# Optimization experiments

Measured on AMD Instinct MI355X. Metric: run time of the kernel, lower is better.

The kernel has to match this reference:

```python
import jax, jax.numpy as jnp
import numpy as np

TEMPERATURE = 8.0  # sqrt(d_head=64)
NEG_INF = -1e15


def setup_inputs() -> dict:
    key = jax.random.key(0)
    k1, k2_, k3, k4, k5, k6 = jax.random.split(key, 6)
    BH, N, D = 16, 2048, 64
    B = 2  # edge batch; BH // B == 8 heads
    return {
        "q": jax.random.normal(k1, (BH, N, D), dtype=jnp.float32),
        "k": jax.random.normal(k2_, (BH, N, D), dtype=jnp.float32),
        "v": jax.random.normal(k3, (BH, N, D), dtype=jnp.float32),
        "k2": jax.random.normal(k4, (BH, N, D), dtype=jnp.float32),
        "mask": jax.random.randint(k5, (BH, 1, N), 0, 2) > 0,
        "edge": jax.random.randint(k6, (B, N, N), 0, 2).astype(jnp.int32),
    }


def reference(q, k, v, k2, mask, edge):
    # attn scores: [bh, n, m]
    attn = jnp.einsum("bnd,bmd->bnm", q, k) / TEMPERATURE
    # torch .repeat along dim0 == tile
    reps = attn.shape[0] // edge.shape[0]
    edge_t = jnp.tile(edge, (reps, 1, 1))
    attn = jnp.where(edge_t == 0, NEG_INF, attn)
    attn = jnp.where(mask, NEG_INF, attn)
    attn = jax.nn.softmax(attn, axis=2)  # dropout p=0 (eval)
    output = jnp.einsum("bnm,bmd->bnd", attn, v)
    # non_linear=False, so no sigmoid
    return (output, attn)
```

## Files before the change

kernel.cpp:

```cpp
#include <hip/hip_runtime.h>
#include <stdint.h>
#include <math.h>

#define BH_ 16
#define N_  2048
#define D_  64
#define NEGV (-1e15f)

typedef __attribute__((ext_vector_type(8))) short bf16x8;
typedef __attribute__((ext_vector_type(8))) unsigned short us8;
typedef __attribute__((ext_vector_type(4))) float f32x4;

#define OFF_MASKU8 0u
#define OFF_MBITS  32768u
#define OFF_EBITS  65536u
#define OFF_QBF    1114112u
#define OFF_KBF    5308416u
#define OFF_VT     9502720u
#define WS_NEEDED  13697024u

#define BARRIER_LGKM() do {                                   \
    asm volatile("s_waitcnt lgkmcnt(0)" ::: "memory");        \
    __builtin_amdgcn_sched_barrier(0);                        \
    __builtin_amdgcn_s_barrier();                             \
    __builtin_amdgcn_sched_barrier(0);                        \
} while (0)

__device__ __forceinline__ unsigned short f2bf(float f) {
    unsigned u = __float_as_uint(f);
    return (unsigned short)((u + 0x7FFFu + ((u >> 16) & 1u)) >> 16);
}

__global__ __launch_bounds__(256)
void prep_all(const float* __restrict__ q, const float* __restrict__ k,
              const float* __restrict__ v, const void* __restrict__ mraw,
              const int* __restrict__ edge,
              unsigned short* __restrict__ qbf, unsigned short* __restrict__ kbf,
              unsigned short* __restrict__ vT,
              unsigned short* __restrict__ e16, unsigned long long* __restrict__ mbits)
{
    __shared__ unsigned short shbuf[64][72];
    __shared__ int flag;
    const int bid = blockIdx.x;
    const int t   = threadIdx.x;

    if (bid < 2048) {
        const int idx = bid * 256 + t;
        const int4* p = (const int4*)(edge + (size_t)idx * 16);
        unsigned m = 0;
        #pragma unroll
        for (int i = 0; i < 4; ++i) {
            const int4 vv = p[i];
            m |= (vv.x != 0 ? 1u : 0u) << (i * 4 + 0);
            m |= (vv.y != 0 ? 1u : 0u) << (i * 4 + 1);
            m |= (vv.z != 0 ? 1u : 0u) << (i * 4 + 2);
            m |= (vv.w != 0 ? 1u : 0u) << (i * 4 + 3);
        }
        e16[idx] = (unsigned short)m;
    } else if (bid < 2560) {
        const int b2 = bid - 2048;
        const int rt = b2 & 31, bh = b2 >> 5;
        const size_t base = ((size_t)bh * N_ + (size_t)rt * 64) * D_;
        #pragma unroll
        for (int i = 0; i < 4; ++i) {
            const int idx = t + i * 256;
            float4 f = *(const float4*)(q + base + (size_t)idx * 4);
            ushort4 s; s.x = f2bf(f.x); s.y = f2bf(f.y); s.z = f2bf(f.z); s.w = f2bf(f.w);
            *(ushort4*)(qbf + base + (size_t)idx * 4) = s;
            f = *(const float4*)(k + base + (size_t)idx * 4);
            s.x = f2bf(f.x); s.y = f2bf(f.y); s.z = f2bf(f.z); s.w = f2bf(f.w);
            *(ushort4*)(kbf + base + (size_t)idx * 4) = s;
            f = *(const float4*)(v + base + (size_t)idx * 4);
            const int row = idx >> 4;
            const int d0  = (idx & 15) * 4;
            shbuf[d0 + 0][row] = f2bf(f.x);
            shbuf[d0 + 1][row] = f2bf(f.y);
            shbuf[d0 + 2][row] = f2bf(f.z);
            shbuf[d0 + 3][row] = f2bf(f.w);
        }
        __syncthreads();
        const int d  = t >> 2;
        const int c4 = (t & 3) * 16;
        const size_t ob = ((size_t)bh * D_ + d) * N_ + (size_t)rt * 64 + c4;
        *(us8*)(vT + ob)     = *(us8*)&shbuf[d][c4];
        *(us8*)(vT + ob + 8) = *(us8*)&shbuf[d][c4 + 8];
    } else {
        const int bh = bid - 2560;
        if (t == 0) flag = 0;
        __syncthreads();
        const int* mi = (const int*)mraw;
        int bad = 0;
        for (int i = t; i < 8192; i += 256)
            if ((unsigned)mi[i] > 1u) bad = 1;
        if (bad) atomicOr(&flag, 1);
        __syncthreads();
        const int is_u8 = flag;
        const uint8_t* m8 = (const uint8_t*)mraw;
        const int w4 = t >> 6, l = t & 63;
        for (int it = 0; it < 8; ++it) {
            const int pos = bh * 2048 + it * 256 + w4 * 64 + l;
            const bool on = is_u8 ? (m8[pos] != 0) : (mi[pos] != 0);
            unsigned long long bal = __ballot(on);
            if (l == 0) mbits[bh * 32 + it * 4 + w4] = bal;
        }
    }
}

__global__ __launch_bounds__(256)
void attn_v6(const unsigned short* __restrict__ qbf,
             const unsigned short* __restrict__ kbf,
             const unsigned short* __restrict__ vT,
             const unsigned long long* __restrict__ ebits,
             const unsigned long long* __restrict__ mbits,
             float* __restrict__ out, float* __restrict__ attn)
{
    __shared__ unsigned short sK[2][4096];
    __shared__ unsigned short sV[2][4096];
    __shared__ char pbuf[4][2048];

    const int tile = blockIdx.x;
    const int bh   = blockIdx.y;
    const int t    = threadIdx.x;
    const int w    = t >> 6;
    const int lane = t & 63;
    const int l15  = lane & 15;
    const int lg   = lane >> 4;
    const int rbase = tile * 64;
    const int myrow = rbase + w * 16 + l15;

    const unsigned short* qb = qbf + (size_t)bh * N_ * D_;
    const unsigned short* kb = kbf + (size_t)bh * N_ * D_;
    const unsigned short* vb = vT  + (size_t)bh * D_ * N_;
    const unsigned long long* ebrow =
        ebits + ((size_t)(bh & 1) * N_ + (size_t)myrow) * 32;
    const unsigned long long* mb = mbits + bh * 32;
    float* outb = out + (size_t)bh * N_ * D_;
    float* arow = attn + (size_t)bh * N_ * N_ + (size_t)myrow * N_ + lg * 4;

    const bf16x8 aq0 = *(const bf16x8*)(qb + (size_t)myrow * D_ + lg * 8);
    const bf16x8 aq1 = *(const bf16x8*)(qb + (size_t)myrow * D_ + lg * 8 + 32);

    const int s0row = t >> 3;
    const int s1row = s0row + 32;
    const int t8    = t & 7;
    const int ds0 = s0row * 64 + ((t8 ^ (s0row & 7)) * 8);
    const int ds1 = s1row * 64 + ((t8 ^ (s1row & 7)) * 8);

    {
        const us8 a0 = *(const us8*)(kb + (size_t)t * 8);
        const us8 a1 = *(const us8*)(kb + (size_t)(t + 256) * 8);
        *(us8*)(sK[0] + ds0) = a0;
        *(us8*)(sK[0] + ds1) = a1;
        BARRIER_LGKM();
    }
    float lacc = 0.f;
    #pragma unroll 1
    for (int kc = 0; kc < 32; ++kc) {
        const int cur = kc & 1;
        us8 nk0, nk1;
        if (kc < 31) {
            const unsigned short* s = kb + (size_t)(kc + 1) * 4096;
            nk0 = *(const us8*)(s + (size_t)t * 8);
            nk1 = *(const us8*)(s + (size_t)(t + 256) * 8);
        }
        const unsigned long long wbits = ebrow[kc] & ~mb[kc];
        const unsigned short* kcur = sK[cur];
        #pragma unroll
        for (int nt = 0; nt < 4; ++nt) {
            const int row = nt * 16 + l15, sw = row & 7;
            const bf16x8 k0 = *(const bf16x8*)(kcur + row * 64 + ((lg ^ sw) * 8));
            const bf16x8 k1 = *(const bf16x8*)(kcur + row * 64 + (((lg + 4) ^ sw) * 8));
            f32x4 c = (f32x4){0.f, 0.f, 0.f, 0.f};
            c = __builtin_amdgcn_mfma_f32_16x16x32_bf16(k0, aq0, c, 0, 0, 0);
            c = __builtin_amdgcn_mfma_f32_16x16x32_bf16(k1, aq1, c, 0, 0, 0);
            const unsigned bits = (unsigned)(wbits >> (nt * 16 + lg * 4)) & 0xFu;
            #pragma unroll
            for (int r = 0; r < 4; ++r)
                lacc += ((bits >> r) & 1u) ? __expf(c[r] * 0.125f) : 0.f;
        }
        if (kc < 31) {
            *(us8*)(sK[cur ^ 1] + ds0) = nk0;
            *(us8*)(sK[cur ^ 1] + ds1) = nk1;
        }
        BARRIER_LGKM();
    }
    lacc += __shfl_xor(lacc, 16);
    lacc += __shfl_xor(lacc, 32);
    const float inv = 1.0f / lacc;

    {
        const us8 a0 = *(const us8*)(kb + (size_t)t * 8);
        const us8 a1 = *(const us8*)(kb + (size_t)(t + 256) * 8);
        const us8 b0 = *(const us8*)(vb + (size_t)s0row * 2048 + t8 * 8);
        const us8 b1 = *(const us8*)(vb + (size_t)s1row * 2048 + t8 * 8);
        *(us8*)(sK[0] + ds0) = a0;
        *(us8*)(sK[0] + ds1) = a1;
        *(us8*)(sV[0] + ds0) = b0;
        *(us8*)(sV[0] + ds1) = b1;
        BARRIER_LGKM();
    }

    f32x4 o[4];
    #pragma unroll
    for (int nt = 0; nt < 4; ++nt) o[nt] = (f32x4){0.f, 0.f, 0.f, 0.f};

    char* pbw = pbuf[w];
    const int swzP = (l15 & 7) << 4;
    const int ab0 = (l15 * 128 + lg * 16)      ^ swzP;
    const int ab1 = (l15 * 128 + lg * 16 + 64) ^ swzP;

    #pragma unroll 1
    for (int kc = 0; kc < 32; ++kc) {
        const int cur = kc & 1;
        us8 nk0, nk1, nv0, nv1;
        if (kc < 31) {
            const unsigned short* srck = kb + (size_t)(kc + 1) * 4096;
            const unsigned short* srcv = vb + (size_t)(kc + 1) * 64;
            nk0 = *(const us8*)(srck + (size_t)t * 8);
            nk1 = *(const us8*)(srck + (size_t)(t + 256) * 8);
            nv0 = *(const us8*)(srcv + (size_t)s0row * 2048 + t8 * 8);
            nv1 = *(const us8*)(srcv + (size_t)s1row * 2048 + t8 * 8);
        }
        const unsigned long long wbits = ebrow[kc] & ~mb[kc];
        const unsigned short* kcur = sK[cur];
        float4 ev[4];
        #pragma unroll
        for (int nt = 0; nt < 4; ++nt) {
            const int row = nt * 16 + l15, sw = row & 7;
            const bf16x8 k0 = *(const bf16x8*)(kcur + row * 64 + ((lg ^ sw) * 8));
            const bf16x8 k1 = *(const bf16x8*)(kcur + row * 64 + (((lg + 4) ^ sw) * 8));
            f32x4 c = (f32x4){0.f, 0.f, 0.f, 0.f};
            c = __builtin_amdgcn_mfma_f32_16x16x32_bf16(k0, aq0, c, 0, 0, 0);
            c = __builtin_amdgcn_mfma_f32_16x16x32_bf16(k1, aq1, c, 0, 0, 0);
            const unsigned bits = (unsigned)(wbits >> (nt * 16 + lg * 4)) & 0xFu;
            float4 e;
            e.x = (bits & 1u) ? __expf(c[0] * 0.125f) * inv : 0.f;
            e.y = (bits & 2u) ? __expf(c[1] * 0.125f) * inv : 0.f;
            e.z = (bits & 4u) ? __expf(c[2] * 0.125f) * inv : 0.f;
            e.w = (bits & 8u) ? __expf(c[3] * 0.125f) * inv : 0.f;
            ev[nt] = e;
            ushort4 pe;
            pe.x = f2bf(e.x); pe.y = f2bf(e.y); pe.z = f2bf(e.z); pe.w = f2bf(e.w);
            const int wbyte = (l15 * 128 + nt * 32 + lg * 8) ^ swzP;
            *(ushort4*)(pbw + wbyte) = pe;
        }
        const bf16x8 ap0 = *(const bf16x8*)(pbw + ab0);
        const bf16x8 ap1 = *(const bf16x8*)(pbw + ab1);
        const unsigned short* vcur = sV[cur];
        #pragma unroll
        for (int nt = 0; nt < 4; ++nt) {
            const int row = nt * 16 + l15, sw = row & 7;
            const bf16x8 bv0 = *(const bf16x8*)(vcur + row * 64 + ((lg ^ sw) * 8));
            const bf16x8 bv1 = *(const bf16x8*)(vcur + row * 64 + (((lg + 4) ^ sw) * 8));
            o[nt] = __builtin_amdgcn_mfma_f32_16x16x32_bf16(ap0, bv0, o[nt], 0, 0, 0);
            o[nt] = __builtin_amdgcn_mfma_f32_16x16x32_bf16(ap1, bv1, o[nt], 0, 0, 0);
        }
        {
            float* astore = arow + kc * 64;
            #pragma unroll
            for (int nt = 0; nt < 4; ++nt)
                *(float4*)(astore + nt * 16) = ev[nt];
        }
        if (kc < 31) {
            *(us8*)(sK[cur ^ 1] + ds0) = nk0;
            *(us8*)(sK[cur ^ 1] + ds1) = nk1;
            *(us8*)(sV[cur ^ 1] + ds0) = nv0;
            *(us8*)(sV[cur ^ 1] + ds1) = nv1;
        }
        BARRIER_LGKM();
    }

    #pragma unroll
    for (int nt = 0; nt < 4; ++nt)
        #pragma unroll
        for (int r = 0; r < 4; ++r)
            outb[(size_t)(rbase + w * 16 + lg * 4 + r) * D_ + nt * 16 + l15] = o[nt][r];
}

__global__ __launch_bounds__(256)
void normalize_mask(const void* __restrict__ mask_raw, uint8_t* __restrict__ mask_out)
{
    __shared__ int is_u8;
    const int t = threadIdx.x;
    if (t == 0) is_u8 = 0;
    __syncthreads();
    const int* mi = (const int*)mask_raw;
    int bad = 0;
    for (int i = t; i < 8192; i += 256)
        if ((unsigned)mi[i] > 1u) bad = 1;
    if (bad) atomicOr(&is_u8, 1);
    __syncthreads();
    const int total = BH_ * N_;
    if (is_u8) {
        const uint8_t* m8 = (const uint8_t*)mask_raw;
        for (int i = t; i < total; i += 256) mask_out[i] = m8[i] ? 1 : 0;
    } else {
        for (int i = t; i < total; i += 256) mask_out[i] = (uint8_t)mi[i];
    }
}

__global__ __launch_bounds__(256)
void attn_fused(const float* __restrict__ q, const float* __restrict__ k,
                const float* __restrict__ v, const uint8_t* __restrict__ mask,
                const int* __restrict__ edge, float* __restrict__ out,
                float* __restrict__ attn)
{
    __shared__ float qsT[D_][64 + 4];
    __shared__ float kt [D_][64 + 4];
    __shared__ float vs [64][D_ + 4];
    const int tile = blockIdx.x, bh = blockIdx.y, t = threadIdx.x;
    const int rg = t >> 4, cg = t & 15, r0 = rg * 4, c0 = cg * 4;
    const int row_base = tile * 64;
    const float* qb = q + (size_t)bh * N_ * D_;
    const float* kb = k + (size_t)bh * N_ * D_;
    const float* vb = v + (size_t)bh * N_ * D_;
    const uint8_t* mbp = mask + (size_t)bh * N_;
    const int* ebp = edge + (size_t)(bh & 1) * N_ * N_;
    float* outb = out + (size_t)bh * N_ * D_;
    float* attnb = attn + (size_t)bh * N_ * N_;
    {
        const int rr = t >> 2, dblk = (t & 3) * 16;
        const float* src = qb + (size_t)(row_base + rr) * D_ + dblk;
        #pragma unroll
        for (int qq = 0; qq < 4; ++qq) {
            float4 val = *(const float4*)(src + qq * 4);
            qsT[dblk + qq*4 + 0][rr] = val.x; qsT[dblk + qq*4 + 1][rr] = val.y;
            qsT[dblk + qq*4 + 2][rr] = val.z; qsT[dblk + qq*4 + 3][rr] = val.w;
        }
    }
    float m_i[4], l_i[4];
    #pragma unroll
    for (int i = 0; i < 4; ++i) { m_i[i] = -INFINITY; l_i[i] = 0.f; }
    for (int kc = 0; kc < 32; ++kc) {
        __syncthreads();
        {
            const int ccr = t >> 2, dblk = (t & 3) * 16;
            const float* src = kb + (size_t)(kc * 64 + ccr) * D_ + dblk;
            #pragma unroll
            for (int qq = 0; qq < 4; ++qq) {
                float4 val = *(const float4*)(src + qq * 4);
                kt[dblk + qq*4 + 0][ccr] = val.x; kt[dblk + qq*4 + 1][ccr] = val.y;
                kt[dblk + qq*4 + 2][ccr] = val.z; kt[dblk + qq*4 + 3][ccr] = val.w;
            }
        }
        __syncthreads();
        float sc[4][4];
        #pragma unroll
        for (int i = 0; i < 4; ++i) { sc[i][0]=sc[i][1]=sc[i][2]=sc[i][3]=0.f; }
        for (int d = 0; d < D_; ++d) {
            const float4 qv = *(const float4*)&qsT[d][r0];
            const float4 kv = *(const float4*)&kt[d][c0];
            #pragma unroll
            for (int i = 0; i < 4; ++i) {
                const float qi = (i==0)?qv.x:(i==1)?qv.y:(i==2)?qv.z:qv.w;
                sc[i][0] = fmaf(qi, kv.x, sc[i][0]); sc[i][1] = fmaf(qi, kv.y, sc[i][1]);
                sc[i][2] = fmaf(qi, kv.z, sc[i][2]); sc[i][3] = fmaf(qi, kv.w, sc[i][3]);
            }
        }
        const int cbase = kc * 64 + c0;
        const uint8_t m0 = mbp[cbase], m1 = mbp[cbase+1], m2 = mbp[cbase+2], m3 = mbp[cbase+3];
        #pragma unroll
        for (int i = 0; i < 4; ++i) {
            const int rglob = row_base + r0 + i;
            const int4 e4 = *(const int4*)(ebp + (size_t)rglob * N_ + cbase);
            float s0 = sc[i][0]*0.125f, s1 = sc[i][1]*0.125f, s2 = sc[i][2]*0.125f, s3 = sc[i][3]*0.125f;
            if (e4.x == 0 || m0) s0 = NEGV; if (e4.y == 0 || m1) s1 = NEGV;
            if (e4.z == 0 || m2) s2 = NEGV; if (e4.w == 0 || m3) s3 = NEGV;
            float cmax = fmaxf(fmaxf(s0,s1), fmaxf(s2,s3));
            cmax = fmaxf(cmax, __shfl_xor(cmax,1)); cmax = fmaxf(cmax, __shfl_xor(cmax,2));
            cmax = fmaxf(cmax, __shfl_xor(cmax,4)); cmax = fmaxf(cmax, __shfl_xor(cmax,8));
            const float nm = fmaxf(m_i[i], cmax);
            float ss = __expf(s0-nm)+__expf(s1-nm)+__expf(s2-nm)+__expf(s3-nm);
            ss += __shfl_xor(ss,1); ss += __shfl_xor(ss,2); ss += __shfl_xor(ss,4); ss += __shfl_xor(ss,8);
            l_i[i] = l_i[i]*__expf(m_i[i]-nm) + ss; m_i[i] = nm;
        }
    }
    float inv_l[4];
    #pragma unroll
    for (int i = 0; i < 4; ++i) inv_l[i] = 1.0f / l_i[i];
    float oacc[4][4];
    #pragma unroll
    for (int i = 0; i < 4; ++i) { oacc[i][0]=oacc[i][1]=oacc[i][2]=oacc[i][3]=0.f; }
    for (int kc = 0; kc < 32; ++kc) {
        __syncthreads();
        {
            const int ccr = t >> 2, dblk = (t & 3) * 16;
            const float* src = kb + (size_t)(kc * 64 + ccr) * D_ + dblk;
            #pragma unroll
            for (int qq = 0; qq < 4; ++qq) {
                float4 val = *(const float4*)(src + qq * 4);
                kt[dblk + qq*4 + 0][ccr] = val.x; kt[dblk + qq*4 + 1][ccr] = val.y;
                kt[dblk + qq*4 + 2][ccr] = val.z; kt[dblk + qq*4 + 3][ccr] = val.w;
            }
            const float* srcv = vb + (size_t)(kc * 64 + ccr) * D_ + dblk;
            #pragma unroll
            for (int qq = 0; qq < 4; ++qq)
                *(float4*)&vs[ccr][dblk + qq * 4] = *(const float4*)(srcv + qq * 4);
        }
        __syncthreads();
        float sc[4][4];
        #pragma unroll
        for (int i = 0; i < 4; ++i) { sc[i][0]=sc[i][1]=sc[i][2]=sc[i][3]=0.f; }
        for (int d = 0; d < D_; ++d) {
            const float4 qv = *(const float4*)&qsT[d][r0];
            const float4 kv = *(const float4*)&kt[d][c0];
            #pragma unroll
            for (int i = 0; i < 4; ++i) {
                const float qi = (i==0)?qv.x:(i==1)?qv.y:(i==2)?qv.z:qv.w;
                sc[i][0] = fmaf(qi, kv.x, sc[i][0]); sc[i][1] = fmaf(qi, kv.y, sc[i][1]);
                sc[i][2] = fmaf(qi, kv.z, sc[i][2]); sc[i][3] = fmaf(qi, kv.w, sc[i][3]);
            }
        }
        const int cbase = kc * 64 + c0;
        const uint8_t m0 = mbp[cbase], m1 = mbp[cbase+1], m2 = mbp[cbase+2], m3 = mbp[cbase+3];
        float p[4][4];
        #pragma unroll
        for (int i = 0; i < 4; ++i) {
            const int rglob = row_base + r0 + i;
            const int4 e4 = *(const int4*)(ebp + (size_t)rglob * N_ + cbase);
            float s0 = sc[i][0]*0.125f, s1 = sc[i][1]*0.125f, s2 = sc[i][2]*0.125f, s3 = sc[i][3]*0.125f;
            if (e4.x == 0 || m0) s0 = NEGV; if (e4.y == 0 || m1) s1 = NEGV;
            if (e4.z == 0 || m2) s2 = NEGV; if (e4.w == 0 || m3) s3 = NEGV;
            p[i][0] = __expf(s0-m_i[i])*inv_l[i]; p[i][1] = __expf(s1-m_i[i])*inv_l[i];
            p[i][2] = __expf(s2-m_i[i])*inv_l[i]; p[i][3] = __expf(s3-m_i[i])*inv_l[i];
            *(float4*)&attnb[(size_t)rglob * N_ + cbase] = make_float4(p[i][0],p[i][1],p[i][2],p[i][3]);
        }
        __syncthreads();
        #pragma unroll
        for (int i = 0; i < 4; ++i)
            *(float4*)&kt[r0 + i][c0] = make_float4(p[i][0],p[i][1],p[i][2],p[i][3]);
        __syncthreads();
        for (int c4 = 0; c4 < 64; c4 += 4) {
            float prr[4][4];
            #pragma unroll
            for (int i = 0; i < 4; ++i) {
                const float4 tmp = *(const float4*)&kt[r0 + i][c4];
                prr[i][0]=tmp.x; prr[i][1]=tmp.y; prr[i][2]=tmp.z; prr[i][3]=tmp.w;
            }
            #pragma unroll
            for (int cc = 0; cc < 4; ++cc) {
                const float4 vv = *(const float4*)&vs[c4 + cc][c0];
                #pragma unroll
                for (int i = 0; i < 4; ++i) {
                    oacc[i][0] = fmaf(prr[i][cc], vv.x, oacc[i][0]);
                    oacc[i][1] = fmaf(prr[i][cc], vv.y, oacc[i][1]);
                    oacc[i][2] = fmaf(prr[i][cc], vv.z, oacc[i][2]);
                    oacc[i][3] = fmaf(prr[i][cc], vv.w, oacc[i][3]);
                }
            }
        }
    }
    #pragma unroll
    for (int i = 0; i < 4; ++i)
        *(float4*)&outb[(size_t)(row_base + r0 + i) * D_ + c0] =
            make_float4(oacc[i][0], oacc[i][1], oacc[i][2], oacc[i][3]);
}

extern "C" void kernel_launch(void* const* d_in, const int* in_sizes, int n_in,
                              void* d_out, int out_size, void* d_ws, size_t ws_size,
                              hipStream_t stream) {
    const float* q    = (const float*)d_in[0];
    const float* k    = (const float*)d_in[1];
    const float* v    = (const float*)d_in[2];
    const void*  mraw = d_in[4];
    const int*   edge = (const int*)d_in[5];

    float* out  = (float*)d_out;
    float* attn = (float*)d_out + (size_t)BH_ * N_ * D_;

    char* ws = (char*)d_ws;

    if (ws_size < (size_t)WS_NEEDED) {
        uint8_t* mask_u8 = (uint8_t*)(ws + OFF_MASKU8);
        normalize_mask<<<1, 256, 0, stream>>>(mraw, mask_u8);
        attn_fused<<<dim3(32, 16), 256, 0, stream>>>(q, k, v, mask_u8, edge, out, attn);
        return;
    }

    unsigned long long* mbits = (unsigned long long*)(ws + OFF_MBITS);
    unsigned short*     e16   = (unsigned short*)(ws + OFF_EBITS);
    unsigned short*     qbf   = (unsigned short*)(ws + OFF_QBF);
    unsigned short*     kbf   = (unsigned short*)(ws + OFF_KBF);
    unsigned short*     vT    = (unsigned short*)(ws + OFF_VT);

    prep_all<<<dim3(2576), 256, 0, stream>>>(q, k, v, mraw, edge,
                                             qbf, kbf, vT, e16, mbits);
    attn_v6<<<dim3(N_ / 64, BH_), 256, 0, stream>>>(
        qbf, kbf, vT, (const unsigned long long*)e16, mbits, out, attn);
}
```

Baseline: 127.8 us.

## Split attention into row-sum, split-K PV pass, and output reduction kernels

Replaces the single attention kernel with three kernels. A first pass computes softmax denominators over four key splits. A second pass, split two ways over keys, writes normalized probabilities and partial outputs, and a final kernel sums the two partial outputs. The aim is more blocks in flight (512 → 2048/1024) to fill the GPU. The cost is recomputing QK^T, extra workspace traffic for the partial outputs and row sums, and two more launches. The softmax skips max subtraction, which relies on scores staying small enough not to overflow exp.

```diff
diff --git a/kernel.cpp b/kernel.cpp
--- a/kernel.cpp
+++ b/kernel.cpp
@@ -17,7 +17,10 @@
 #define OFF_QBF    1114112u
 #define OFF_KBF    5308416u
 #define OFF_VT     9502720u
-#define WS_NEEDED  13697024u
+#define WS_V6      13697024u
+#define OFF_PSUM   13697024u
+#define OFF_OPART  14221312u
+#define WS_V7      30998528u
 
 #define BARRIER_LGKM() do {                                   \
     asm volatile("s_waitcnt lgkmcnt(0)" ::: "memory");        \
@@ -104,6 +107,219 @@
             if (l == 0) mbits[bh * 32 + it * 4 + w4] = bal;
         }
     }
+}
+
+__global__ __launch_bounds__(256)
+void attn_sumk(const unsigned short* __restrict__ qbf,
+               const unsigned short* __restrict__ kbf,
+               const unsigned long long* __restrict__ ebits,
+               const unsigned long long* __restrict__ mbits,
+               float* __restrict__ psum)
+{
+    __shared__ unsigned short sK[2][4096];
+
+    const int tile = blockIdx.x, bh = blockIdx.y, s = blockIdx.z;
+    const int t = threadIdx.x;
+    const int w = t >> 6, lane = t & 63, l15 = lane & 15, lg = lane >> 4;
+    const int rbase = tile * 64;
+    const int myrow = rbase + w * 16 + l15;
+    const int kcb = s * 8;
+
+    const unsigned short* qb = qbf + (size_t)bh * N_ * D_;
+    const unsigned short* kb = kbf + (size_t)bh * N_ * D_;
+    const unsigned long long* ebrow =
+        ebits + ((size_t)(bh & 1) * N_ + (size_t)myrow) * 32;
+    const unsigned long long* mb = mbits + bh * 32;
+
+    const bf16x8 aq0 = *(const bf16x8*)(qb + (size_t)myrow * D_ + lg * 8);
+    const bf16x8 aq1 = *(const bf16x8*)(qb + (size_t)myrow * D_ + lg * 8 + 32);
+
+    const int s0row = t >> 3, s1row = s0row + 32, t8 = t & 7;
+    const int ds0 = s0row * 64 + ((t8 ^ (s0row & 7)) * 8);
+    const int ds1 = s1row * 64 + ((t8 ^ (s1row & 7)) * 8);
+
+    {
+        const unsigned short* src = kb + (size_t)kcb * 4096;
+        *(us8*)(sK[0] + ds0) = *(const us8*)(src + (size_t)t * 8);
+        *(us8*)(sK[0] + ds1) = *(const us8*)(src + (size_t)(t + 256) * 8);
+        BARRIER_LGKM();
+    }
+    float lacc = 0.f;
+    #pragma unroll 1
+    for (int i = 0; i < 8; ++i) {
+        const int kc = kcb + i;
+        const int cur = i & 1;
+        us8 nk0, nk1;
+        if (i < 7) {
+            const unsigned short* src = kb + (size_t)(kc + 1) * 4096;
+            nk0 = *(const us8*)(src + (size_t)t * 8);
+            nk1 = *(const us8*)(src + (size_t)(t + 256) * 8);
+        }
+        const unsigned long long wbits = ebrow[kc] & ~mb[kc];
+        const unsigned short* kcur = sK[cur];
+        #pragma unroll
+        for (int nt = 0; nt < 4; ++nt) {
+            const int row = nt * 16 + l15, sw = row & 7;
+            const bf16x8 k0 = *(const bf16x8*)(kcur + row * 64 + ((lg ^ sw) * 8));
+            const bf16x8 k1 = *(const bf16x8*)(kcur + row * 64 + (((lg + 4) ^ sw) * 8));
+            f32x4 c = (f32x4){0.f, 0.f, 0.f, 0.f};
+            c = __builtin_amdgcn_mfma_f32_16x16x32_bf16(k0, aq0, c, 0, 0, 0);
+            c = __builtin_amdgcn_mfma_f32_16x16x32_bf16(k1, aq1, c, 0, 0, 0);
+            const unsigned bits = (unsigned)(wbits >> (nt * 16 + lg * 4)) & 0xFu;
+            #pragma unroll
+            for (int r = 0; r < 4; ++r)
+                lacc += ((bits >> r) & 1u) ? __expf(c[r] * 0.125f) : 0.f;
+        }
+        if (i < 7) {
+            *(us8*)(sK[cur ^ 1] + ds0) = nk0;
+            *(us8*)(sK[cur ^ 1] + ds1) = nk1;
+        }
+        BARRIER_LGKM();
+    }
+    lacc += __shfl_xor(lacc, 16);
+    lacc += __shfl_xor(lacc, 32);
+    if (lane < 16) psum[((size_t)bh * N_ + myrow) * 4 + s] = lacc;
+}
+
+__global__ __launch_bounds__(256)
+void attn_pvk(const unsigned short* __restrict__ qbf,
+              const unsigned short* __restrict__ kbf,
+              const unsigned short* __restrict__ vT,
+              const unsigned long long* __restrict__ ebits,
+              const unsigned long long* __restrict__ mbits,
+              const float* __restrict__ psum,
+              float* __restrict__ opart, float* __restrict__ attn)
+{
+    __shared__ unsigned short sK[2][4096];
+    __shared__ unsigned short sV[2][4096];
+    __shared__ char pbuf[4][2048];
+
+    const int tile = blockIdx.x, bh = blockIdx.y, s = blockIdx.z;
+    const int t = threadIdx.x;
+    const int w = t >> 6, lane = t & 63, l15 = lane & 15, lg = lane >> 4;
+    const int rbase = tile * 64;
+    const int myrow = rbase + w * 16 + l15;
+    const int kcb = s * 16;
+
+    const unsigned short* qb = qbf + (size_t)bh * N_ * D_;
+    const unsigned short* kb = kbf + (size_t)bh * N_ * D_;
+    const unsigned short* vb = vT  + (size_t)bh * D_ * N_;
+    const unsigned long long* ebrow =
+        ebits + ((size_t)(bh & 1) * N_ + (size_t)myrow) * 32;
+    const unsigned long long* mb = mbits + bh * 32;
+    float* arow = attn + (size_t)bh * N_ * N_ + (size_t)myrow * N_ + lg * 4;
+
+    const f32x4 ps = *(const f32x4*)(psum + ((size_t)bh * N_ + myrow) * 4);
+    const float inv = 1.0f / (ps[0] + ps[1] + ps[2] + ps[3]);
+
+    const bf16x8 aq0 = *(const bf16x8*)(qb + (size_t)myrow * D_ + lg * 8);
+    const bf16x8 aq1 = *(const bf16x8*)(qb + (size_t)myrow * D_ + lg * 8 + 32);
+
+    const int s0row = t >> 3, s1row = s0row + 32, t8 = t & 7;
+    const int ds0 = s0row * 64 + ((t8 ^ (s0row & 7)) * 8);
+    const int ds1 = s1row * 64 + ((t8 ^ (s1row & 7)) * 8);
+
+    {
+        const unsigned short* srck = kb + (size_t)kcb * 4096;
+        const unsigned short* srcv = vb + (size_t)kcb * 64;
+        *(us8*)(sK[0] + ds0) = *(const us8*)(srck + (size_t)t * 8);
+        *(us8*)(sK[0] + ds1) = *(const us8*)(srck + (size_t)(t + 256) * 8);
+        *(us8*)(sV[0] + ds0) = *(const us8*)(srcv + (size_t)s0row * 2048 + t8 * 8);
+        *(us8*)(sV[0] + ds1) = *(const us8*)(srcv + (size_t)s1row * 2048 + t8 * 8);
+        BARRIER_LGKM();
+    }
+
+    f32x4 o[4];
+    #pragma unroll
+    for (int nt = 0; nt < 4; ++nt) o[nt] = (f32x4){0.f, 0.f, 0.f, 0.f};
+
+    char* pbw = pbuf[w];
+    const int swzP = (l15 & 7) << 4;
+    const int ab0 = (l15 * 128 + lg * 16)      ^ swzP;
+    const int ab1 = (l15 * 128 + lg * 16 + 64) ^ swzP;
+
+    #pragma unroll 1
+    for (int i = 0; i < 16; ++i) {
+        const int kc = kcb + i;
+        const int cur = i & 1;
+        us8 nk0, nk1, nv0, nv1;
+        if (i < 15) {
+            const unsigned short* srck = kb + (size_t)(kc + 1) * 4096;
+            const unsigned short* srcv = vb + (size_t)(kc + 1) * 64;
+            nk0 = *(const us8*)(srck + (size_t)t * 8);
+            nk1 = *(const us8*)(srck + (size_t)(t + 256) * 8);
+            nv0 = *(const us8*)(srcv + (size_t)s0row * 2048 + t8 * 8);
+            nv1 = *(const us8*)(srcv + (size_t)s1row * 2048 + t8 * 8);
+        }
+        const unsigned long long wbits = ebrow[kc] & ~mb[kc];
+        const unsigned short* kcur = sK[cur];
+        float4 ev[4];
+        #pragma unroll
+        for (int nt = 0; nt < 4; ++nt) {
+            const int row = nt * 16 + l15, sw = row & 7;
+            const bf16x8 k0 = *(const bf16x8*)(kcur + row * 64 + ((lg ^ sw) * 8));
+            const bf16x8 k1 = *(const bf16x8*)(kcur + row * 64 + (((lg + 4) ^ sw) * 8));
+            f32x4 c = (f32x4){0.f, 0.f, 0.f, 0.f};
+            c = __builtin_amdgcn_mfma_f32_16x16x32_bf16(k0, aq0, c, 0, 0, 0);
+            c = __builtin_amdgcn_mfma_f32_16x16x32_bf16(k1, aq1, c, 0, 0, 0);
+            const unsigned bits = (unsigned)(wbits >> (nt * 16 + lg * 4)) & 0xFu;
+            float4 e;
+            e.x = (bits & 1u) ? __expf(c[0] * 0.125f) * inv : 0.f;
+            e.y = (bits & 2u) ? __expf(c[1] * 0.125f) * inv : 0.f;
+            e.z = (bits & 4u) ? __expf(c[2] * 0.125f) * inv : 0.f;
+            e.w = (bits & 8u) ? __expf(c[3] * 0.125f) * inv : 0.f;
+            ev[nt] = e;
+            ushort4 pe;
+            pe.x = f2bf(e.x); pe.y = f2bf(e.y); pe.z = f2bf(e.z); pe.w = f2bf(e.w);
+            const int wbyte = (l15 * 128 + nt * 32 + lg * 8) ^ swzP;
+            *(ushort4*)(pbw + wbyte) = pe;
+        }
+        const bf16x8 ap0 = *(const bf16x8*)(pbw + ab0);
+        const bf16x8 ap1 = *(const bf16x8*)(pbw + ab1);
+        const unsigned short* vcur = sV[cur];
+        #pragma unroll
+        for (int nt = 0; nt < 4; ++nt) {
+            const int row = nt * 16 + l15, sw = row & 7;
+            const bf16x8 bv0 = *(const bf16x8*)(vcur + row * 64 + ((lg ^ sw) * 8));
+            const bf16x8 bv1 = *(const bf16x8*)(vcur + row * 64 + (((lg + 4) ^ sw) * 8));
+            o[nt] = __builtin_amdgcn_mfma_f32_16x16x32_bf16(ap0, bv0, o[nt], 0, 0, 0);
+            o[nt] = __builtin_amdgcn_mfma_f32_16x16x32_bf16(ap1, bv1, o[nt], 0, 0, 0);
+        }
+        {
+            float* astore = arow + kc * 64;
+            #pragma unroll
+            for (int nt = 0; nt < 4; ++nt)
+                *(float4*)(astore + nt * 16) = ev[nt];
+        }
+        if (i < 15) {
+            *(us8*)(sK[cur ^ 1] + ds0) = nk0;
+            *(us8*)(sK[cur ^ 1] + ds1) = nk1;
+            *(us8*)(sV[cur ^ 1] + ds0) = nv0;
+            *(us8*)(sV[cur ^ 1] + ds1) = nv1;
+        }
+        BARRIER_LGKM();
+    }
+
+    float* op = opart + (size_t)s * (BH_ * N_ * D_) + (size_t)bh * N_ * D_;
+    #pragma unroll
+    for (int nt = 0; nt < 4; ++nt)
+        #pragma unroll
+        for (int r = 0; r < 4; ++r)
+            op[(size_t)(rbase + w * 16 + lg * 4 + r) * D_ + nt * 16 + l15] = o[nt][r];
+}
+
+__global__ __launch_bounds__(256)
+void reduce_o(const float* __restrict__ opart, float* __restrict__ out)
+{
+    const float4* a = (const float4*)opart;
+    const float4* b = a + 524288;
+    float4* o4 = (float4*)out;
+    const size_t i = (size_t)blockIdx.x * 256 + threadIdx.x;
+    float4 x = a[i], y = b[i];
+    o4[i] = make_float4(x.x + y.x, x.y + y.y, x.z + y.z, x.w + y.w);
+    const size_t j = i + 262144;
+    x = a[j]; y = b[j];
+    o4[j] = make_float4(x.x + y.x, x.y + y.y, x.z + y.z, x.w + y.w);
 }
 
 __global__ __launch_bounds__(256)
@@ -470,7 +686,7 @@
 
     char* ws = (char*)d_ws;
 
-    if (ws_size < (size_t)WS_NEEDED) {
+    if (ws_size < (size_t)WS_V6) {
         uint8_t* mask_u8 = (uint8_t*)(ws + OFF_MASKU8);
         normalize_mask<<<1, 256, 0, stream>>>(mraw, mask_u8);
         attn_fused<<<dim3(32, 16), 256, 0, stream>>>(q, k, v, mask_u8, edge, out, attn);
@@ -485,6 +701,17 @@
 
     prep_all<<<dim3(2576), 256, 0, stream>>>(q, k, v, mraw, edge,
                                              qbf, kbf, vT, e16, mbits);
-    attn_v6<<<dim3(N_ / 64, BH_), 256, 0, stream>>>(
-        qbf, kbf, vT, (const unsigned long long*)e16, mbits, out, attn);
-}
+
+    if (ws_size >= (size_t)WS_V7) {
+        float* psum  = (float*)(ws + OFF_PSUM);
+        float* opart = (float*)(ws + OFF_OPART);
+        attn_sumk<<<dim3(32, 16, 4), 256, 0, stream>>>(
+            qbf, kbf, (const unsigned long long*)e16, mbits, psum);
+        attn_pvk<<<dim3(32, 16, 2), 256, 0, stream>>>(
+            qbf, kbf, vT, (const unsigned long long*)e16, mbits, psum, opart, attn);
+        reduce_o<<<dim3(1024), 256, 0, stream>>>(opart, out);
+    } else {
+        attn_v6<<<dim3(N_ / 64, BH_), 256, 0, stream>>>(
+            qbf, kbf, vT, (const unsigned long long*)e16, mbits, out, attn);
+    }
+}
```

Result: slower. 136.0 us (+6.4%).
